# Kernel optimization log

Measured on AMD Instinct MI355X. Metric: run time of the kernel, lower is better.

## Reference

```python
import jax, jax.numpy as jnp
import numpy as np

N_NODES = 50000
N_EDGES = 800000
F_IN, F_HID, F_OUT = 128, 256, 64


def setup_inputs() -> dict:
    key = jax.random.key(0)
    ks = jax.random.split(key, 8)
    return {
        "x": jax.random.normal(ks[0], (N_NODES, F_IN), dtype=jnp.float32),
        "edge_index": jax.random.randint(ks[1], (2, N_EDGES), 0, N_NODES, dtype=jnp.int32),
        "W_l1": jax.random.normal(ks[2], (F_IN, F_HID), dtype=jnp.float32) * (1.0 / np.sqrt(F_IN)),
        "W_r1": jax.random.normal(ks[3], (F_IN, F_HID), dtype=jnp.float32) * (1.0 / np.sqrt(F_IN)),
        "b1": jnp.zeros((F_HID,), dtype=jnp.float32),
        "W_l2": jax.random.normal(ks[4], (F_HID, F_OUT), dtype=jnp.float32) * (1.0 / np.sqrt(F_HID)),
        "W_r2": jax.random.normal(ks[5], (F_HID, F_OUT), dtype=jnp.float32) * (1.0 / np.sqrt(F_HID)),
        "b2": jnp.zeros((F_OUT,), dtype=jnp.float32),
    }


def _sage_conv(x, src, dst, W_l, W_r, b):
    # PyG SAGEConv, mean aggregation:
    #   out = mean_{j in N(i)} x_j @ W_l + b + x_i @ W_r
    n = x.shape[0]
    msgs = x[src]                                              # [E, F] gather
    agg_sum = jax.ops.segment_sum(msgs, dst, num_segments=n)   # [N, F] scatter-add
    deg = jax.ops.segment_sum(jnp.ones_like(dst, dtype=x.dtype), dst, num_segments=n)
    agg = agg_sum / jnp.maximum(deg, 1.0)[:, None]             # isolated nodes -> 0
    return agg @ W_l + x @ W_r + b


def reference(x, edge_index, W_l1, W_r1, b1, W_l2, W_r2, b2):
    src, dst = edge_index[0], edge_index[1]
    # layer 1 + relu (dropout is identity in eval mode)
    h = jax.nn.relu(_sage_conv(x, src, dst, W_l1, W_r1, b1))
    # layer 2, multi_class=False -> sigmoid
    out = jax.nn.sigmoid(_sage_conv(h, src, dst, W_l2, W_r2, b2))
    return out
```

## Files before the change

kernel.cpp:

```cpp
#include <hip/hip_runtime.h>
#include <cstdint>
#include <cstddef>


#define N_NODES 50000
#define N_EDGES 800000
#define F_IN 128
#define F_HID 256
#define F_OUT 64
#define CAP 48
#define BINW 128

#define NBIN ((N_NODES + BINW - 1) / BINW)
#define EPB 4096
#define NBLK_A ((N_EDGES + EPB - 1) / EPB)
#define CHUNK 32

#define PREP_TOTAL (N_NODES * 64 + 256 * 256 + 128 * 256)
#define NBLK_PREP ((PREP_TOTAL + 255) / 256)

typedef __attribute__((ext_vector_type(8))) short bf16x8;
typedef __attribute__((ext_vector_type(4))) float f32x4;
typedef __attribute__((ext_vector_type(2))) float f32x2;

__device__ inline unsigned short f2bf(float f) {
    unsigned int u = __float_as_uint(f);
    u += 0x7fffu + ((u >> 16) & 1u);
    return (unsigned short)(u >> 16);
}
__device__ inline unsigned int pack_bf2(float lo, float hi) {
    return (unsigned int)f2bf(lo) | ((unsigned int)f2bf(hi) << 16);
}
__device__ inline float bf_lo(unsigned int u) { return __uint_as_float(u << 16); }
__device__ inline float bf_hi(unsigned int u) { return __uint_as_float(u & 0xffff0000u); }

__device__ inline void gload16(const short* g, short* l) {
    __builtin_amdgcn_global_load_lds(
        (const __attribute__((address_space(1))) void*)g,
        (__attribute__((address_space(3))) void*)l, 16, 0, 0);
}

__global__ __launch_bounds__(256) void binprep_kernel(
    const int* __restrict__ src, const int* __restrict__ dst, int* __restrict__ blkbincnt,
    unsigned int* __restrict__ chunks, const float* __restrict__ x,
    const float* __restrict__ Wl1, const float* __restrict__ Wr1, const float* __restrict__ Wl2,
    const float* __restrict__ Wr2, unsigned int* __restrict__ xbf,
    unsigned short* __restrict__ xq16, short* __restrict__ Bt1, short* __restrict__ Bt2) {
    __shared__ unsigned int ls[NBIN * CHUNK];
    __shared__ int hist[NBIN];
    const int bid = blockIdx.x;
    const int tid = threadIdx.x;
    if (bid < NBLK_A) {
        for (int i = tid; i < NBIN; i += 256) hist[i] = 0;
        __syncthreads();
        const int base = bid * EPB;
        const int nloc = min(EPB, N_EDGES - base);
        for (int j = tid; j < nloc; j += 256) {
            int e = base + j;
            int d = dst[e];
            int s = src[e];
            int bin = d >> 7;
            int p = atomicAdd(&hist[bin], 1);
            if (p < CHUNK)
                ls[bin * CHUNK + p] = ((unsigned int)(d & (BINW - 1)) << 16) | (unsigned int)s;
        }
        __syncthreads();
        for (int i = tid; i < NBIN; i += 256) blkbincnt[bid * NBIN + i] = hist[i];
        unsigned int* outp = &chunks[(size_t)bid * NBIN * CHUNK];
        for (int idx = tid; idx < NBIN * CHUNK; idx += 256) {
            int bin = idx >> 5, i = idx & 31;
            if (i < min(hist[bin], CHUNK)) outp[idx] = ls[idx];
        }
        return;
    }
    int i = (bid - NBLK_A) * 256 + tid;
    if (i < N_NODES * 64) {
        int row = i >> 6, c = i & 63;
        float2 f = *reinterpret_cast<const float2*>(&x[(size_t)row * F_IN + 2 * c]);
        xbf[(size_t)row * 64 + c] = pack_bf2(f.x, f.y);
        xq16[(size_t)row * 64 + c] =
            (unsigned short)(__builtin_amdgcn_cvt_pk_fp8_f32(f.x, f.y, 0, false) & 0xffff);
        return;
    }
    i -= N_NODES * 64;
    if (i < 256 * 256) {
        int k = i >> 8, n = i & 255;
        float v = (k < 128) ? Wl1[k * 256 + n] : Wr1[(k - 128) * 256 + n];
        Bt1[n * 256 + k] = (short)f2bf(v);
        return;
    }
    i -= 256 * 256;
    if (i < 128 * 256) {
        int k = i >> 7, n = i & 127;
        float v = (n < 64) ? Wl2[k * 64 + n] : Wr2[k * 64 + (n - 64)];
        Bt2[n * 256 + k] = (short)f2bf(v);
    }
}

__global__ __launch_bounds__(1024) void bpart_agg_kernel(const unsigned int* __restrict__ chunks,
                                                         const int* __restrict__ blkbincnt,
                                                         int* __restrict__ cnt,
                                                         unsigned short* __restrict__ slots,
                                                         const unsigned int* __restrict__ xq,
                                                         unsigned int* __restrict__ aggx) {
    __shared__ int cur[BINW];
    __shared__ unsigned short ls[BINW * CAP];
    __shared__ int ccnt[NBLK_A];
    const int bin = blockIdx.x;
    const int tid = threadIdx.x;
    if (tid < BINW) cur[tid] = 0;
    for (int i = tid; i < NBLK_A; i += 1024) ccnt[i] = min(blkbincnt[i * NBIN + bin], CHUNK);
    __syncthreads();
    for (int idx = tid; idx < NBLK_A * CHUNK; idx += 1024) {
        int blk = idx >> 5, i = idx & 31;
        if (i < ccnt[blk]) {
            unsigned int pk = chunks[((size_t)blk * NBIN + bin) * CHUNK + i];
            int dl = pk >> 16;
            int p = atomicAdd(&cur[dl], 1);
            if (p < CAP) ls[dl * CAP + p] = (unsigned short)(pk & 0xffffu);
        }
    }
    __syncthreads();
    if (tid < BINW) {
        int node = bin * BINW + tid;
        if (node < N_NODES) cnt[node] = cur[tid];
    }
    const uint4* lsv = reinterpret_cast<const uint4*>(ls);
    uint4* gv = reinterpret_cast<uint4*>(&slots[(size_t)bin * BINW * CAP]);
    for (int i = tid; i < BINW * 6; i += 1024) {
        int row = i / 6;
        if (bin * BINW + row < N_NODES) gv[i] = lsv[i];
    }
    const int grp = tid >> 4;
    const int t = tid & 15;
    const uint2* xq2 = reinterpret_cast<const uint2*>(xq);
    for (int nb = 0; nb < BINW / 64; ++nb) {
        const int local = nb * 64 + grp;
        const int node = bin * BINW + local;
        if (node >= N_NODES) continue;
        const int deg = cur[local];
        const int n = min(deg, CAP);
        const unsigned short* sl = &ls[local * CAP];
        float a[8];
#pragma unroll
        for (int q = 0; q < 8; ++q) a[q] = 0.f;
        int j = 0;
        for (; j + 16 <= n; j += 16) {
            uint4 sv0 = *reinterpret_cast<const uint4*>(&sl[j]);
            uint4 sv1 = *reinterpret_cast<const uint4*>(&sl[j + 8]);
            int s[16];
            s[0] = sv0.x & 0xffff; s[1] = sv0.x >> 16;
            s[2] = sv0.y & 0xffff; s[3] = sv0.y >> 16;
            s[4] = sv0.z & 0xffff; s[5] = sv0.z >> 16;
            s[6] = sv0.w & 0xffff; s[7] = sv0.w >> 16;
            s[8] = sv1.x & 0xffff; s[9] = sv1.x >> 16;
            s[10] = sv1.y & 0xffff; s[11] = sv1.y >> 16;
            s[12] = sv1.z & 0xffff; s[13] = sv1.z >> 16;
            s[14] = sv1.w & 0xffff; s[15] = sv1.w >> 16;
            uint2 u[16];
#pragma unroll
            for (int q = 0; q < 16; ++q) u[q] = xq2[(size_t)s[q] * 16 + t];
#pragma unroll
            for (int q = 0; q < 16; ++q) {
                f32x2 p0 = __builtin_amdgcn_cvt_pk_f32_fp8((int)u[q].x, false);
                f32x2 p1 = __builtin_amdgcn_cvt_pk_f32_fp8((int)u[q].x, true);
                f32x2 p2 = __builtin_amdgcn_cvt_pk_f32_fp8((int)u[q].y, false);
                f32x2 p3 = __builtin_amdgcn_cvt_pk_f32_fp8((int)u[q].y, true);
                a[0] += p0.x; a[1] += p0.y; a[2] += p1.x; a[3] += p1.y;
                a[4] += p2.x; a[5] += p2.y; a[6] += p3.x; a[7] += p3.y;
            }
        }
        for (; j + 8 <= n; j += 8) {
            uint4 sv = *reinterpret_cast<const uint4*>(&sl[j]);
            int s[8];
            s[0] = sv.x & 0xffff; s[1] = sv.x >> 16;
            s[2] = sv.y & 0xffff; s[3] = sv.y >> 16;
            s[4] = sv.z & 0xffff; s[5] = sv.z >> 16;
            s[6] = sv.w & 0xffff; s[7] = sv.w >> 16;
            uint2 u[8];
#pragma unroll
            for (int q = 0; q < 8; ++q) u[q] = xq2[(size_t)s[q] * 16 + t];
#pragma unroll
            for (int q = 0; q < 8; ++q) {
                f32x2 p0 = __builtin_amdgcn_cvt_pk_f32_fp8((int)u[q].x, false);
                f32x2 p1 = __builtin_amdgcn_cvt_pk_f32_fp8((int)u[q].x, true);
                f32x2 p2 = __builtin_amdgcn_cvt_pk_f32_fp8((int)u[q].y, false);
                f32x2 p3 = __builtin_amdgcn_cvt_pk_f32_fp8((int)u[q].y, true);
                a[0] += p0.x; a[1] += p0.y; a[2] += p1.x; a[3] += p1.y;
                a[4] += p2.x; a[5] += p2.y; a[6] += p3.x; a[7] += p3.y;
            }
        }
        for (; j + 4 <= n; j += 4) {
            uint2 sv = *reinterpret_cast<const uint2*>(&sl[j]);
            int s[4];
            s[0] = sv.x & 0xffff; s[1] = sv.x >> 16;
            s[2] = sv.y & 0xffff; s[3] = sv.y >> 16;
            uint2 u[4];
#pragma unroll
            for (int q = 0; q < 4; ++q) u[q] = xq2[(size_t)s[q] * 16 + t];
#pragma unroll
            for (int q = 0; q < 4; ++q) {
                f32x2 p0 = __builtin_amdgcn_cvt_pk_f32_fp8((int)u[q].x, false);
                f32x2 p1 = __builtin_amdgcn_cvt_pk_f32_fp8((int)u[q].x, true);
                f32x2 p2 = __builtin_amdgcn_cvt_pk_f32_fp8((int)u[q].y, false);
                f32x2 p3 = __builtin_amdgcn_cvt_pk_f32_fp8((int)u[q].y, true);
                a[0] += p0.x; a[1] += p0.y; a[2] += p1.x; a[3] += p1.y;
                a[4] += p2.x; a[5] += p2.y; a[6] += p3.x; a[7] += p3.y;
            }
        }
        for (; j < n; ++j) {
            uint2 u = xq2[(size_t)sl[j] * 16 + t];
            f32x2 p0 = __builtin_amdgcn_cvt_pk_f32_fp8((int)u.x, false);
            f32x2 p1 = __builtin_amdgcn_cvt_pk_f32_fp8((int)u.x, true);
            f32x2 p2 = __builtin_amdgcn_cvt_pk_f32_fp8((int)u.y, false);
            f32x2 p3 = __builtin_amdgcn_cvt_pk_f32_fp8((int)u.y, true);
            a[0] += p0.x; a[1] += p0.y; a[2] += p1.x; a[3] += p1.y;
            a[4] += p2.x; a[5] += p2.y; a[6] += p3.x; a[7] += p3.y;
        }
        float scale = (deg > 0) ? 1.0f / (float)deg : 0.0f;
        uint4 o;
        o.x = pack_bf2(a[0] * scale, a[1] * scale);
        o.y = pack_bf2(a[2] * scale, a[3] * scale);
        o.z = pack_bf2(a[4] * scale, a[5] * scale);
        o.w = pack_bf2(a[6] * scale, a[7] * scale);
        *reinterpret_cast<uint4*>(&aggx[(size_t)node * 64 + t * 4]) = o;
    }
}

#define LDH 264
__global__ __launch_bounds__(256) void gemm_fused_kernel(const short* __restrict__ Aagg,
                                                         const short* __restrict__ Aself,
                                                         const short* __restrict__ Bt1,
                                                         const short* __restrict__ Bt2,
                                                         const float* __restrict__ b1,
                                                         unsigned char* __restrict__ grq,
                                                         short* __restrict__ grR) {
    __shared__ short smem[64 * LDH + 128 * 64];
    short* As = smem;
    short* Bs1 = smem + 64 * 64;
    short* Hs = smem;
    short* Bs2 = smem + 64 * LDH;

    const int tid = threadIdx.x;
    const int lane = tid & 63;
    const int wave = tid >> 6;
    const int quad = lane >> 4;
    const int l16 = lane & 15;
    const int m0 = blockIdx.x * 64;
    const int M = N_NODES;

    const int srow = lane >> 3;
    const int sswz = (lane & 7) ^ srow;

    f32x4 acc[4][4];
#pragma unroll
    for (int i = 0; i < 4; ++i)
#pragma unroll
        for (int j = 0; j < 4; ++j) acc[i][j] = (f32x4)(0.0f);

    const int wn1 = wave * 64;

    for (int k0 = 0; k0 < 256; k0 += 64) {
        const short* Asrc = (k0 < 128) ? Aagg : Aself;
        const int kbase = k0 & 127;
#pragma unroll
        for (int j = 0; j < 2; ++j) {
            int i = wave * 2 + j;
            int row = i * 8 + srow;
            int gm = m0 + row;
            gm = (gm < M) ? gm : (M - 1);
            gload16(Asrc + (size_t)gm * 128 + kbase + (sswz << 3), As + i * 512);
        }
#pragma unroll
        for (int j = 0; j < 8; ++j) {
            int i = wave + j * 4;
            int row = i * 8 + srow;
            gload16(Bt1 + (size_t)row * 256 + k0 + (sswz << 3), Bs1 + i * 512);
        }
        __syncthreads();
#pragma unroll
        for (int kk = 0; kk < 64; kk += 32) {
            const int sw = (((kk >> 3) + quad) ^ (l16 & 7)) << 3;
            bf16x8 af[4], bfr[4];
#pragma unroll
            for (int mi = 0; mi < 4; ++mi)
                af[mi] = *reinterpret_cast<const bf16x8*>(&As[(mi * 16 + l16) * 64 + sw]);
#pragma unroll
            for (int ni = 0; ni < 4; ++ni)
                bfr[ni] = *reinterpret_cast<const bf16x8*>(
                    &Bs1[(wn1 + ni * 16 + l16) * 64 + sw]);
#pragma unroll
            for (int mi = 0; mi < 4; ++mi)
#pragma unroll
                for (int ni = 0; ni < 4; ++ni)
                    acc[mi][ni] = __builtin_amdgcn_mfma_f32_16x16x32_bf16(af[mi], bfr[ni],
                                                                          acc[mi][ni], 0, 0, 0);
        }
        __syncthreads();
    }

    float biasv[4];
#pragma unroll
    for (int ni = 0; ni < 4; ++ni) biasv[ni] = b1[wn1 + ni * 16 + l16];
#pragma unroll
    for (int mi = 0; mi < 4; ++mi)
#pragma unroll
        for (int reg = 0; reg < 4; ++reg) {
            int row = mi * 16 + quad * 4 + reg;
#pragma unroll
            for (int ni = 0; ni < 4; ++ni) {
                float v = fmaxf(acc[mi][ni][reg] + biasv[ni], 0.0f);
                Hs[row * LDH + wn1 + ni * 16 + l16] = (short)f2bf(v);
            }
        }
    __syncthreads();

    f32x4 acc2[2][4];
#pragma unroll
    for (int i = 0; i < 2; ++i)
#pragma unroll
        for (int j = 0; j < 4; ++j) acc2[i][j] = (f32x4)(0.0f);

    const int wm2 = (wave >> 1) * 32;
    const int wn2 = (wave & 1) * 64;

    for (int k0 = 0; k0 < 256; k0 += 64) {
#pragma unroll
        for (int j = 0; j < 4; ++j) {
            int i = wave + j * 4;
            int row = i * 8 + srow;
            gload16(Bt2 + (size_t)row * 256 + k0 + (sswz << 3), Bs2 + i * 512);
        }
        __syncthreads();
#pragma unroll
        for (int kk = 0; kk < 64; kk += 32) {
            const int sw = (((kk >> 3) + quad) ^ (l16 & 7)) << 3;
            bf16x8 af[2], bfr[4];
#pragma unroll
            for (int mi = 0; mi < 2; ++mi)
                af[mi] = *reinterpret_cast<const bf16x8*>(
                    &Hs[(wm2 + mi * 16 + l16) * LDH + k0 + kk + quad * 8]);
#pragma unroll
            for (int ni = 0; ni < 4; ++ni)
                bfr[ni] = *reinterpret_cast<const bf16x8*>(
                    &Bs2[(wn2 + ni * 16 + l16) * 64 + sw]);
#pragma unroll
            for (int mi = 0; mi < 2; ++mi)
#pragma unroll
                for (int ni = 0; ni < 4; ++ni)
                    acc2[mi][ni] = __builtin_amdgcn_mfma_f32_16x16x32_bf16(af[mi], bfr[ni],
                                                                           acc2[mi][ni], 0, 0, 0);
        }
        __syncthreads();
    }

#pragma unroll
    for (int mi = 0; mi < 2; ++mi)
#pragma unroll
        for (int reg = 0; reg < 4; ++reg) {
            int gm = m0 + wm2 + mi * 16 + quad * 4 + reg;
            if (gm >= M) continue;
#pragma unroll
            for (int ni = 0; ni < 4; ++ni) {
                int gn = wn2 + ni * 16 + l16;
                float v = acc2[mi][ni][reg];
                if (gn < 64) {
                    grq[(size_t)gm * 64 + gn] =
                        (unsigned char)(__builtin_amdgcn_cvt_pk_fp8_f32(v, v, 0, false) & 0xff);
                } else {
                    grR[(size_t)gm * 64 + (gn - 64)] = (short)f2bf(v);
                }
            }
        }
}

__global__ __launch_bounds__(256) void final_kernel(const unsigned int* __restrict__ grq,
                                                    const unsigned int* __restrict__ grRu,
                                                    const int* __restrict__ cnt,
                                                    const unsigned short* __restrict__ slots,
                                                    const float* __restrict__ b2,
                                                    float* __restrict__ out) {
    const int node = blockIdx.x * 32 + (threadIdx.x >> 3);
    const int t = threadIdx.x & 7;
    if (node >= N_NODES) return;
    const int deg = cnt[node];
    const int n = min(deg, CAP);
    const unsigned short* sl = &slots[(size_t)node * CAP];
    const uint2* g2 = reinterpret_cast<const uint2*>(grq);
    float a[8];
#pragma unroll
    for (int q = 0; q < 8; ++q) a[q] = 0.f;
    int j = 0;
    for (; j + 16 <= n; j += 16) {
        uint4 sv0 = *reinterpret_cast<const uint4*>(&sl[j]);
        uint4 sv1 = *reinterpret_cast<const uint4*>(&sl[j + 8]);
        int s[16];
        s[0] = sv0.x & 0xffff; s[1] = sv0.x >> 16;
        s[2] = sv0.y & 0xffff; s[3] = sv0.y >> 16;
        s[4] = sv0.z & 0xffff; s[5] = sv0.z >> 16;
        s[6] = sv0.w & 0xffff; s[7] = sv0.w >> 16;
        s[8] = sv1.x & 0xffff; s[9] = sv1.x >> 16;
        s[10] = sv1.y & 0xffff; s[11] = sv1.y >> 16;
        s[12] = sv1.z & 0xffff; s[13] = sv1.z >> 16;
        s[14] = sv1.w & 0xffff; s[15] = sv1.w >> 16;
        uint2 u[16];
#pragma unroll
        for (int q = 0; q < 16; ++q) u[q] = g2[(size_t)s[q] * 8 + t];
#pragma unroll
        for (int q = 0; q < 16; ++q) {
            f32x2 p0 = __builtin_amdgcn_cvt_pk_f32_fp8((int)u[q].x, false);
            f32x2 p1 = __builtin_amdgcn_cvt_pk_f32_fp8((int)u[q].x, true);
            f32x2 p2 = __builtin_amdgcn_cvt_pk_f32_fp8((int)u[q].y, false);
            f32x2 p3 = __builtin_amdgcn_cvt_pk_f32_fp8((int)u[q].y, true);
            a[0] += p0.x; a[1] += p0.y; a[2] += p1.x; a[3] += p1.y;
            a[4] += p2.x; a[5] += p2.y; a[6] += p3.x; a[7] += p3.y;
        }
    }
    for (; j + 8 <= n; j += 8) {
        uint4 sv = *reinterpret_cast<const uint4*>(&sl[j]);
        int s[8];
        s[0] = sv.x & 0xffff; s[1] = sv.x >> 16;
        s[2] = sv.y & 0xffff; s[3] = sv.y >> 16;
        s[4] = sv.z & 0xffff; s[5] = sv.z >> 16;
        s[6] = sv.w & 0xffff; s[7] = sv.w >> 16;
        uint2 u[8];
#pragma unroll
        for (int q = 0; q < 8; ++q) u[q] = g2[(size_t)s[q] * 8 + t];
#pragma unroll
        for (int q = 0; q < 8; ++q) {
            f32x2 p0 = __builtin_amdgcn_cvt_pk_f32_fp8((int)u[q].x, false);
            f32x2 p1 = __builtin_amdgcn_cvt_pk_f32_fp8((int)u[q].x, true);
            f32x2 p2 = __builtin_amdgcn_cvt_pk_f32_fp8((int)u[q].y, false);
            f32x2 p3 = __builtin_amdgcn_cvt_pk_f32_fp8((int)u[q].y, true);
            a[0] += p0.x; a[1] += p0.y; a[2] += p1.x; a[3] += p1.y;
            a[4] += p2.x; a[5] += p2.y; a[6] += p3.x; a[7] += p3.y;
        }
    }
    for (; j + 4 <= n; j += 4) {
        uint2 sv = *reinterpret_cast<const uint2*>(&sl[j]);
        int s[4];
        s[0] = sv.x & 0xffff; s[1] = sv.x >> 16;
        s[2] = sv.y & 0xffff; s[3] = sv.y >> 16;
        uint2 u[4];
#pragma unroll
        for (int q = 0; q < 4; ++q) u[q] = g2[(size_t)s[q] * 8 + t];
#pragma unroll
        for (int q = 0; q < 4; ++q) {
            f32x2 p0 = __builtin_amdgcn_cvt_pk_f32_fp8((int)u[q].x, false);
            f32x2 p1 = __builtin_amdgcn_cvt_pk_f32_fp8((int)u[q].x, true);
            f32x2 p2 = __builtin_amdgcn_cvt_pk_f32_fp8((int)u[q].y, false);
            f32x2 p3 = __builtin_amdgcn_cvt_pk_f32_fp8((int)u[q].y, true);
            a[0] += p0.x; a[1] += p0.y; a[2] += p1.x; a[3] += p1.y;
            a[4] += p2.x; a[5] += p2.y; a[6] += p3.x; a[7] += p3.y;
        }
    }
    for (; j < n; ++j) {
        uint2 u = g2[(size_t)sl[j] * 8 + t];
        f32x2 p0 = __builtin_amdgcn_cvt_pk_f32_fp8((int)u.x, false);
        f32x2 p1 = __builtin_amdgcn_cvt_pk_f32_fp8((int)u.x, true);
        f32x2 p2 = __builtin_amdgcn_cvt_pk_f32_fp8((int)u.y, false);
        f32x2 p3 = __builtin_amdgcn_cvt_pk_f32_fp8((int)u.y, true);
        a[0] += p0.x; a[1] += p0.y; a[2] += p1.x; a[3] += p1.y;
        a[4] += p2.x; a[5] += p2.y; a[6] += p3.x; a[7] += p3.y;
    }
    float scale = (deg > 0) ? 1.0f / (float)deg : 0.0f;
    uint4 r = *reinterpret_cast<const uint4*>(&grRu[(size_t)node * 32 + t * 4]);
    float4 bv0 = *reinterpret_cast<const float4*>(&b2[t * 8]);
    float4 bv1 = *reinterpret_cast<const float4*>(&b2[t * 8 + 4]);
    float v0 = a[0] * scale + bf_lo(r.x) + bv0.x;
    float v1 = a[1] * scale + bf_hi(r.x) + bv0.y;
    float v2 = a[2] * scale + bf_lo(r.y) + bv0.z;
    float v3 = a[3] * scale + bf_hi(r.y) + bv0.w;
    float v4 = a[4] * scale + bf_lo(r.z) + bv1.x;
    float v5 = a[5] * scale + bf_hi(r.z) + bv1.y;
    float v6 = a[6] * scale + bf_lo(r.w) + bv1.z;
    float v7 = a[7] * scale + bf_hi(r.w) + bv1.w;
    float4 o0, o1;
    o0.x = 1.0f / (1.0f + __expf(-v0));
    o0.y = 1.0f / (1.0f + __expf(-v1));
    o0.z = 1.0f / (1.0f + __expf(-v2));
    o0.w = 1.0f / (1.0f + __expf(-v3));
    o1.x = 1.0f / (1.0f + __expf(-v4));
    o1.y = 1.0f / (1.0f + __expf(-v5));
    o1.z = 1.0f / (1.0f + __expf(-v6));
    o1.w = 1.0f / (1.0f + __expf(-v7));
    *reinterpret_cast<float4*>(&out[(size_t)node * 64 + t * 8]) = o0;
    *reinterpret_cast<float4*>(&out[(size_t)node * 64 + t * 8 + 4]) = o1;
}


extern "C" void kernel_launch(void* const* d_in, const int* in_sizes, int n_in,
                              void* d_out, int out_size, void* d_ws, size_t ws_size,
                              hipStream_t stream) {
    const float* x   = (const float*)d_in[0];
    const int* ei    = (const int*)d_in[1];
    const float* Wl1 = (const float*)d_in[2];
    const float* Wr1 = (const float*)d_in[3];
    const float* b1  = (const float*)d_in[4];
    const float* Wl2 = (const float*)d_in[5];
    const float* Wr2 = (const float*)d_in[6];
    const float* b2  = (const float*)d_in[7];
    float* out       = (float*)d_out;

    const int* src = ei;
    const int* dst = ei + N_EDGES;

    char* p = (char*)d_ws;
    auto alloc = [&](size_t bytes) {
        char* r = p;
        p += (bytes + 255) & ~(size_t)255;
        return (void*)r;
    };
    int* cnt              = (int*)alloc((size_t)N_NODES * 4);
    unsigned short* slots = (unsigned short*)alloc((size_t)NBIN * BINW * CAP * 2);
    int* blkbincnt        = (int*)alloc((size_t)NBLK_A * NBIN * 4);
    unsigned int* chunks  = (unsigned int*)alloc((size_t)NBLK_A * NBIN * CHUNK * 4);
    unsigned int* xbf     = (unsigned int*)alloc((size_t)N_NODES * 64 * 4);
    unsigned short* xq16  = (unsigned short*)alloc((size_t)N_NODES * 64 * 2);
    unsigned int* aggx    = (unsigned int*)alloc((size_t)N_NODES * 64 * 4);
    unsigned char* grq    = (unsigned char*)alloc((size_t)N_NODES * 64);
    short* grR            = (short*)alloc((size_t)N_NODES * 64 * 2);
    short* Bt1            = (short*)alloc((size_t)256 * 256 * 2);
    short* Bt2            = (short*)alloc((size_t)128 * 256 * 2);
    (void)ws_size;

    binprep_kernel<<<NBLK_A + NBLK_PREP, 256, 0, stream>>>(src, dst, blkbincnt, chunks, x, Wl1,
                                                           Wr1, Wl2, Wr2, xbf, xq16, Bt1, Bt2);
    bpart_agg_kernel<<<NBIN, 1024, 0, stream>>>(chunks, blkbincnt, cnt, slots,
                                                (const unsigned int*)xq16, aggx);

    gemm_fused_kernel<<<(N_NODES + 63) / 64, 256, 0, stream>>>(
        (const short*)aggx, (const short*)xbf, Bt1, Bt2, b1, grq, grR);

    final_kernel<<<(N_NODES + 31) / 32, 256, 0, stream>>>((const unsigned int*)grq,
                                                          (const unsigned int*)grR, cnt, slots,
                                                          b2, out);
}
```

Before: 165.3 us.

## Split fused partition/prep and partition/aggregate kernels into separate launches

Splits the combined edge-binning and feature-prep kernel into two kernels, and splits the bin-partition kernel from the layer-1 neighbor aggregation. Aggregation now runs as its own kernel with 16 nodes per 256-thread block, reading slot lists from global memory instead of LDS. The aim is finer-grained parallelism for aggregation, instead of 391 large 1024-thread blocks that each handle 128 nodes. In exchange it adds two kernel launches and a global round trip for the slot lists and counts.

```diff
diff --git a/kernel.cpp b/kernel.cpp
--- a/kernel.cpp
+++ b/kernel.cpp
@@ -40,40 +40,46 @@
         (__attribute__((address_space(3))) void*)l, 16, 0, 0);
 }
 
-__global__ __launch_bounds__(256) void binprep_kernel(
-    const int* __restrict__ src, const int* __restrict__ dst, int* __restrict__ blkbincnt,
-    unsigned int* __restrict__ chunks, const float* __restrict__ x,
-    const float* __restrict__ Wl1, const float* __restrict__ Wr1, const float* __restrict__ Wl2,
-    const float* __restrict__ Wr2, unsigned int* __restrict__ xbf,
-    unsigned short* __restrict__ xq16, short* __restrict__ Bt1, short* __restrict__ Bt2) {
+__global__ __launch_bounds__(256) void part_kernel(const int* __restrict__ src,
+                                                   const int* __restrict__ dst,
+                                                   int* __restrict__ blkbincnt,
+                                                   unsigned int* __restrict__ chunks) {
     __shared__ unsigned int ls[NBIN * CHUNK];
     __shared__ int hist[NBIN];
     const int bid = blockIdx.x;
     const int tid = threadIdx.x;
-    if (bid < NBLK_A) {
-        for (int i = tid; i < NBIN; i += 256) hist[i] = 0;
-        __syncthreads();
-        const int base = bid * EPB;
-        const int nloc = min(EPB, N_EDGES - base);
-        for (int j = tid; j < nloc; j += 256) {
-            int e = base + j;
-            int d = dst[e];
-            int s = src[e];
-            int bin = d >> 7;
-            int p = atomicAdd(&hist[bin], 1);
-            if (p < CHUNK)
-                ls[bin * CHUNK + p] = ((unsigned int)(d & (BINW - 1)) << 16) | (unsigned int)s;
-        }
-        __syncthreads();
-        for (int i = tid; i < NBIN; i += 256) blkbincnt[bid * NBIN + i] = hist[i];
-        unsigned int* outp = &chunks[(size_t)bid * NBIN * CHUNK];
-        for (int idx = tid; idx < NBIN * CHUNK; idx += 256) {
-            int bin = idx >> 5, i = idx & 31;
-            if (i < min(hist[bin], CHUNK)) outp[idx] = ls[idx];
-        }
-        return;
-    }
-    int i = (bid - NBLK_A) * 256 + tid;
+    for (int i = tid; i < NBIN; i += 256) hist[i] = 0;
+    __syncthreads();
+    const int base = bid * EPB;
+    const int nloc = min(EPB, N_EDGES - base);
+    for (int j = tid; j < nloc; j += 256) {
+        int e = base + j;
+        int d = dst[e];
+        int s = src[e];
+        int bin = d >> 7;
+        int p = atomicAdd(&hist[bin], 1);
+        if (p < CHUNK)
+            ls[bin * CHUNK + p] = ((unsigned int)(d & (BINW - 1)) << 16) | (unsigned int)s;
+    }
+    __syncthreads();
+    for (int i = tid; i < NBIN; i += 256) blkbincnt[bid * NBIN + i] = hist[i];
+    unsigned int* outp = &chunks[(size_t)bid * NBIN * CHUNK];
+    for (int idx = tid; idx < NBIN * CHUNK; idx += 256) {
+        int bin = idx >> 5, i = idx & 31;
+        if (i < min(hist[bin], CHUNK)) outp[idx] = ls[idx];
+    }
+}
+
+__global__ __launch_bounds__(256) void prep_kernel(const float* __restrict__ x,
+                                                   const float* __restrict__ Wl1,
+                                                   const float* __restrict__ Wr1,
+                                                   const float* __restrict__ Wl2,
+                                                   const float* __restrict__ Wr2,
+                                                   unsigned int* __restrict__ xbf,
+                                                   unsigned short* __restrict__ xq16,
+                                                   short* __restrict__ Bt1,
+                                                   short* __restrict__ Bt2) {
+    int i = blockIdx.x * 256 + threadIdx.x;
     if (i < N_NODES * 64) {
         int row = i >> 6, c = i & 63;
         float2 f = *reinterpret_cast<const float2*>(&x[(size_t)row * F_IN + 2 * c]);
@@ -97,12 +103,10 @@
     }
 }
 
-__global__ __launch_bounds__(1024) void bpart_agg_kernel(const unsigned int* __restrict__ chunks,
-                                                         const int* __restrict__ blkbincnt,
-                                                         int* __restrict__ cnt,
-                                                         unsigned short* __restrict__ slots,
-                                                         const unsigned int* __restrict__ xq,
-                                                         unsigned int* __restrict__ aggx) {
+__global__ __launch_bounds__(1024) void bpart_kernel(const unsigned int* __restrict__ chunks,
+                                                     const int* __restrict__ blkbincnt,
+                                                     int* __restrict__ cnt,
+                                                     unsigned short* __restrict__ slots) {
     __shared__ int cur[BINW];
     __shared__ unsigned short ls[BINW * CAP];
     __shared__ int ccnt[NBLK_A];
@@ -131,100 +135,102 @@
         int row = i / 6;
         if (bin * BINW + row < N_NODES) gv[i] = lsv[i];
     }
-    const int grp = tid >> 4;
-    const int t = tid & 15;
+}
+
+__global__ __launch_bounds__(256) void agg1_kernel(const int* __restrict__ cnt,
+                                                   const unsigned short* __restrict__ slots,
+                                                   const unsigned int* __restrict__ xq,
+                                                   unsigned int* __restrict__ aggx) {
+    const int node = blockIdx.x * 16 + (threadIdx.x >> 4);
+    const int t = threadIdx.x & 15;
+    if (node >= N_NODES) return;
+    const int deg = cnt[node];
+    const int n = min(deg, CAP);
+    const unsigned short* sl = &slots[(size_t)node * CAP];
     const uint2* xq2 = reinterpret_cast<const uint2*>(xq);
-    for (int nb = 0; nb < BINW / 64; ++nb) {
-        const int local = nb * 64 + grp;
-        const int node = bin * BINW + local;
-        if (node >= N_NODES) continue;
-        const int deg = cur[local];
-        const int n = min(deg, CAP);
-        const unsigned short* sl = &ls[local * CAP];
-        float a[8];
-#pragma unroll
-        for (int q = 0; q < 8; ++q) a[q] = 0.f;
-        int j = 0;
-        for (; j + 16 <= n; j += 16) {
-            uint4 sv0 = *reinterpret_cast<const uint4*>(&sl[j]);
-            uint4 sv1 = *reinterpret_cast<const uint4*>(&sl[j + 8]);
-            int s[16];
-            s[0] = sv0.x & 0xffff; s[1] = sv0.x >> 16;
-            s[2] = sv0.y & 0xffff; s[3] = sv0.y >> 16;
-            s[4] = sv0.z & 0xffff; s[5] = sv0.z >> 16;
-            s[6] = sv0.w & 0xffff; s[7] = sv0.w >> 16;
-            s[8] = sv1.x & 0xffff; s[9] = sv1.x >> 16;
-            s[10] = sv1.y & 0xffff; s[11] = sv1.y >> 16;
-            s[12] = sv1.z & 0xffff; s[13] = sv1.z >> 16;
-            s[14] = sv1.w & 0xffff; s[15] = sv1.w >> 16;
-            uint2 u[16];
-#pragma unroll
-            for (int q = 0; q < 16; ++q) u[q] = xq2[(size_t)s[q] * 16 + t];
-#pragma unroll
-            for (int q = 0; q < 16; ++q) {
-                f32x2 p0 = __builtin_amdgcn_cvt_pk_f32_fp8((int)u[q].x, false);
-                f32x2 p1 = __builtin_amdgcn_cvt_pk_f32_fp8((int)u[q].x, true);
-                f32x2 p2 = __builtin_amdgcn_cvt_pk_f32_fp8((int)u[q].y, false);
-                f32x2 p3 = __builtin_amdgcn_cvt_pk_f32_fp8((int)u[q].y, true);
-                a[0] += p0.x; a[1] += p0.y; a[2] += p1.x; a[3] += p1.y;
-                a[4] += p2.x; a[5] += p2.y; a[6] += p3.x; a[7] += p3.y;
-            }
-        }
-        for (; j + 8 <= n; j += 8) {
-            uint4 sv = *reinterpret_cast<const uint4*>(&sl[j]);
-            int s[8];
-            s[0] = sv.x & 0xffff; s[1] = sv.x >> 16;
-            s[2] = sv.y & 0xffff; s[3] = sv.y >> 16;
-            s[4] = sv.z & 0xffff; s[5] = sv.z >> 16;
-            s[6] = sv.w & 0xffff; s[7] = sv.w >> 16;
-            uint2 u[8];
-#pragma unroll
-            for (int q = 0; q < 8; ++q) u[q] = xq2[(size_t)s[q] * 16 + t];
-#pragma unroll
-            for (int q = 0; q < 8; ++q) {
-                f32x2 p0 = __builtin_amdgcn_cvt_pk_f32_fp8((int)u[q].x, false);
-                f32x2 p1 = __builtin_amdgcn_cvt_pk_f32_fp8((int)u[q].x, true);
-                f32x2 p2 = __builtin_amdgcn_cvt_pk_f32_fp8((int)u[q].y, false);
-                f32x2 p3 = __builtin_amdgcn_cvt_pk_f32_fp8((int)u[q].y, true);
-                a[0] += p0.x; a[1] += p0.y; a[2] += p1.x; a[3] += p1.y;
-                a[4] += p2.x; a[5] += p2.y; a[6] += p3.x; a[7] += p3.y;
-            }
-        }
-        for (; j + 4 <= n; j += 4) {
-            uint2 sv = *reinterpret_cast<const uint2*>(&sl[j]);
-            int s[4];
-            s[0] = sv.x & 0xffff; s[1] = sv.x >> 16;
-            s[2] = sv.y & 0xffff; s[3] = sv.y >> 16;
-            uint2 u[4];
-#pragma unroll
-            for (int q = 0; q < 4; ++q) u[q] = xq2[(size_t)s[q] * 16 + t];
-#pragma unroll
-            for (int q = 0; q < 4; ++q) {
-                f32x2 p0 = __builtin_amdgcn_cvt_pk_f32_fp8((int)u[q].x, false);
-                f32x2 p1 = __builtin_amdgcn_cvt_pk_f32_fp8((int)u[q].x, true);
-                f32x2 p2 = __builtin_amdgcn_cvt_pk_f32_fp8((int)u[q].y, false);
-                f32x2 p3 = __builtin_amdgcn_cvt_pk_f32_fp8((int)u[q].y, true);
-                a[0] += p0.x; a[1] += p0.y; a[2] += p1.x; a[3] += p1.y;
-                a[4] += p2.x; a[5] += p2.y; a[6] += p3.x; a[7] += p3.y;
-            }
-        }
-        for (; j < n; ++j) {
-            uint2 u = xq2[(size_t)sl[j] * 16 + t];
-            f32x2 p0 = __builtin_amdgcn_cvt_pk_f32_fp8((int)u.x, false);
-            f32x2 p1 = __builtin_amdgcn_cvt_pk_f32_fp8((int)u.x, true);
-            f32x2 p2 = __builtin_amdgcn_cvt_pk_f32_fp8((int)u.y, false);
-            f32x2 p3 = __builtin_amdgcn_cvt_pk_f32_fp8((int)u.y, true);
+    float a[8];
+#pragma unroll
+    for (int q = 0; q < 8; ++q) a[q] = 0.f;
+    int j = 0;
+    for (; j + 16 <= n; j += 16) {
+        uint4 sv0 = *reinterpret_cast<const uint4*>(&sl[j]);
+        uint4 sv1 = *reinterpret_cast<const uint4*>(&sl[j + 8]);
+        int s[16];
+        s[0] = sv0.x & 0xffff; s[1] = sv0.x >> 16;
+        s[2] = sv0.y & 0xffff; s[3] = sv0.y >> 16;
+        s[4] = sv0.z & 0xffff; s[5] = sv0.z >> 16;
+        s[6] = sv0.w & 0xffff; s[7] = sv0.w >> 16;
+        s[8] = sv1.x & 0xffff; s[9] = sv1.x >> 16;
+        s[10] = sv1.y & 0xffff; s[11] = sv1.y >> 16;
+        s[12] = sv1.z & 0xffff; s[13] = sv1.z >> 16;
+        s[14] = sv1.w & 0xffff; s[15] = sv1.w >> 16;
+        uint2 u[16];
+#pragma unroll
+        for (int q = 0; q < 16; ++q) u[q] = xq2[(size_t)s[q] * 16 + t];
+#pragma unroll
+        for (int q = 0; q < 16; ++q) {
+            f32x2 p0 = __builtin_amdgcn_cvt_pk_f32_fp8((int)u[q].x, false);
+            f32x2 p1 = __builtin_amdgcn_cvt_pk_f32_fp8((int)u[q].x, true);
+            f32x2 p2 = __builtin_amdgcn_cvt_pk_f32_fp8((int)u[q].y, false);
+            f32x2 p3 = __builtin_amdgcn_cvt_pk_f32_fp8((int)u[q].y, true);
             a[0] += p0.x; a[1] += p0.y; a[2] += p1.x; a[3] += p1.y;
             a[4] += p2.x; a[5] += p2.y; a[6] += p3.x; a[7] += p3.y;
         }
-        float scale = (deg > 0) ? 1.0f / (float)deg : 0.0f;
-        uint4 o;
-        o.x = pack_bf2(a[0] * scale, a[1] * scale);
-        o.y = pack_bf2(a[2] * scale, a[3] * scale);
-        o.z = pack_bf2(a[4] * scale, a[5] * scale);
-        o.w = pack_bf2(a[6] * scale, a[7] * scale);
-        *reinterpret_cast<uint4*>(&aggx[(size_t)node * 64 + t * 4]) = o;
-    }
+    }
+    for (; j + 8 <= n; j += 8) {
+        uint4 sv = *reinterpret_cast<const uint4*>(&sl[j]);
+        int s[8];
+        s[0] = sv.x & 0xffff; s[1] = sv.x >> 16;
+        s[2] = sv.y & 0xffff; s[3] = sv.y >> 16;
+        s[4] = sv.z & 0xffff; s[5] = sv.z >> 16;
+        s[6] = sv.w & 0xffff; s[7] = sv.w >> 16;
+        uint2 u[8];
+#pragma unroll
+        for (int q = 0; q < 8; ++q) u[q] = xq2[(size_t)s[q] * 16 + t];
+#pragma unroll
+        for (int q = 0; q < 8; ++q) {
+            f32x2 p0 = __builtin_amdgcn_cvt_pk_f32_fp8((int)u[q].x, false);
+            f32x2 p1 = __builtin_amdgcn_cvt_pk_f32_fp8((int)u[q].x, true);
+            f32x2 p2 = __builtin_amdgcn_cvt_pk_f32_fp8((int)u[q].y, false);
+            f32x2 p3 = __builtin_amdgcn_cvt_pk_f32_fp8((int)u[q].y, true);
+            a[0] += p0.x; a[1] += p0.y; a[2] += p1.x; a[3] += p1.y;
+            a[4] += p2.x; a[5] += p2.y; a[6] += p3.x; a[7] += p3.y;
+        }
+    }
+    for (; j + 4 <= n; j += 4) {
+        uint2 sv = *reinterpret_cast<const uint2*>(&sl[j]);
+        int s[4];
+        s[0] = sv.x & 0xffff; s[1] = sv.x >> 16;
+        s[2] = sv.y & 0xffff; s[3] = sv.y >> 16;
+        uint2 u[4];
+#pragma unroll
+        for (int q = 0; q < 4; ++q) u[q] = xq2[(size_t)s[q] * 16 + t];
+#pragma unroll
+        for (int q = 0; q < 4; ++q) {
+            f32x2 p0 = __builtin_amdgcn_cvt_pk_f32_fp8((int)u[q].x, false);
+            f32x2 p1 = __builtin_amdgcn_cvt_pk_f32_fp8((int)u[q].x, true);
+            f32x2 p2 = __builtin_amdgcn_cvt_pk_f32_fp8((int)u[q].y, false);
+            f32x2 p3 = __builtin_amdgcn_cvt_pk_f32_fp8((int)u[q].y, true);
+            a[0] += p0.x; a[1] += p0.y; a[2] += p1.x; a[3] += p1.y;
+            a[4] += p2.x; a[5] += p2.y; a[6] += p3.x; a[7] += p3.y;
+        }
+    }
+    for (; j < n; ++j) {
+        uint2 u = xq2[(size_t)sl[j] * 16 + t];
+        f32x2 p0 = __builtin_amdgcn_cvt_pk_f32_fp8((int)u.x, false);
+        f32x2 p1 = __builtin_amdgcn_cvt_pk_f32_fp8((int)u.x, true);
+        f32x2 p2 = __builtin_amdgcn_cvt_pk_f32_fp8((int)u.y, false);
+        f32x2 p3 = __builtin_amdgcn_cvt_pk_f32_fp8((int)u.y, true);
+        a[0] += p0.x; a[1] += p0.y; a[2] += p1.x; a[3] += p1.y;
+        a[4] += p2.x; a[5] += p2.y; a[6] += p3.x; a[7] += p3.y;
+    }
+    float scale = (deg > 0) ? 1.0f / (float)deg : 0.0f;
+    uint4 o;
+    o.x = pack_bf2(a[0] * scale, a[1] * scale);
+    o.y = pack_bf2(a[2] * scale, a[3] * scale);
+    o.z = pack_bf2(a[4] * scale, a[5] * scale);
+    o.w = pack_bf2(a[6] * scale, a[7] * scale);
+    *reinterpret_cast<uint4*>(&aggx[(size_t)node * 64 + t * 4]) = o;
 }
 
 #define LDH 264
@@ -524,10 +530,11 @@
     short* Bt2            = (short*)alloc((size_t)128 * 256 * 2);
     (void)ws_size;
 
-    binprep_kernel<<<NBLK_A + NBLK_PREP, 256, 0, stream>>>(src, dst, blkbincnt, chunks, x, Wl1,
-                                                           Wr1, Wl2, Wr2, xbf, xq16, Bt1, Bt2);
-    bpart_agg_kernel<<<NBIN, 1024, 0, stream>>>(chunks, blkbincnt, cnt, slots,
-                                                (const unsigned int*)xq16, aggx);
+    part_kernel<<<NBLK_A, 256, 0, stream>>>(src, dst, blkbincnt, chunks);
+    prep_kernel<<<NBLK_PREP, 256, 0, stream>>>(x, Wl1, Wr1, Wl2, Wr2, xbf, xq16, Bt1, Bt2);
+    bpart_kernel<<<NBIN, 1024, 0, stream>>>(chunks, blkbincnt, cnt, slots);
+    agg1_kernel<<<(N_NODES + 15) / 16, 256, 0, stream>>>(cnt, slots,
+                                                         (const unsigned int*)xq16, aggx);
 
     gemm_fused_kernel<<<(N_NODES + 63) / 64, 256, 0, stream>>>(
         (const short*)aggx, (const short*)xbf, Bt1, Bt2, b1, grq, grR);
```

After: 171.4 us. +3.7%, slower.
